# Optimization experiments

Hardware: AMD Instinct MI355X
Metric: run time of the kernel (lower is better)

Reference implementation:

```python
import jax, jax.numpy as jnp
import numpy as np

B, NP, C_IN, H = 8, 6250, 512, 256   # graphs, nodes/graph, in-feat, hidden
EPG = 100000                          # edges per graph
K = 5000                              # ceil(0.8 * NP) kept by TopKPooling
H3 = 3 * H


def setup_inputs() -> dict:
    key = jax.random.key(0)
    ks = jax.random.split(key, 16)
    N, E = B * NP, B * EPG
    x = jax.random.normal(ks[0], (N, C_IN), jnp.float32)
    offs = (jnp.arange(E) // EPG) * NP  # keep edges inside their graph
    src = jax.random.randint(ks[1], (E,), 0, NP) + offs
    dst = jax.random.randint(ks[2], (E,), 0, NP) + offs
    edge_index = jnp.stack([src, dst]).astype(jnp.int64)
    edge_attr = jax.random.uniform(ks[3], (E,), jnp.float32)
    batch = jnp.repeat(jnp.arange(B), NP).astype(jnp.int64)
    s = 0.05
    W1 = jax.random.normal(ks[4], (C_IN, H), jnp.float32) * s
    b1 = jnp.zeros((H,), jnp.float32)
    W2 = jax.random.normal(ks[5], (H, H), jnp.float32) * s
    b2 = jnp.zeros((H,), jnp.float32)
    pw = jax.random.normal(ks[6], (H3,), jnp.float32) * s   # TopKPooling attn vector
    lw1 = jax.random.normal(ks[7], (H3 * 2, H), jnp.float32) * s
    lb1 = jnp.zeros((H,), jnp.float32)
    lw2 = jax.random.normal(ks[8], (H, H // 2), jnp.float32) * s
    lb2 = jnp.zeros((H // 2,), jnp.float32)
    lw3 = jax.random.normal(ks[9], (H // 2, 3), jnp.float32) * s
    lb3 = jnp.zeros((3,), jnp.float32)
    return {"x": x, "edge_index": edge_index, "edge_attr": edge_attr, "batch": batch,
            "W1": W1, "b1": b1, "W2": W2, "b2": b2, "pw": pw,
            "lw1": lw1, "lb1": lb1, "lw2": lw2, "lb2": lb2, "lw3": lw3, "lb3": lb3}


def _gcn(x, W, b, src, dst, ew, n):
    xw = x @ W
    deg = jnp.zeros((n,), xw.dtype).at[dst].add(ew) + 1.0
    dinv = jax.lax.rsqrt(deg)
    norm = dinv[src] * ew * dinv[dst]
    out = jnp.zeros_like(xw).at[dst].add(norm[:, None] * xw[src])
    return out + (dinv * dinv)[:, None] * xw + b


def reference(x, edge_index, edge_attr, batch, W1, b1, W2, b2, pw,
              lw1, lb1, lw2, lb2, lw3, lb3):
    N = x.shape[0]
    src, dst = edge_index[0], edge_index[1]
    x1 = jax.nn.relu(_gcn(x, W1, b1, src, dst, edge_attr, N))
    x2 = jax.nn.relu(_gcn(x1, W2, b2, src, dst, edge_attr, N))
    x3 = jax.nn.relu(_gcn(x2, W2, b2, src, dst, edge_attr, N))  # conv2 reused (as in source)
    cat_x = jnp.concatenate([x1, x2, x3], axis=1)               # [N, 3H]
    # TopKPooling: score = sigmoid((x . w) / ||w||), keep top-K per graph, scale by score
    score = jax.nn.sigmoid((cat_x @ pw) / jnp.linalg.norm(pw))   # [N]
    sc = score.reshape(B, NP)
    topv, topi = jax.lax.top_k(sc, K)                            # [B, K]
    xg = cat_x.reshape(B, NP, H3)
    sel = jnp.take_along_axis(xg, topi[:, :, None], axis=1) * topv[:, :, None]  # [B, K, 3H]
    readout = jnp.concatenate([sel.mean(axis=1), sel.max(axis=1)], axis=1)      # [B, 6H]
    h = jax.nn.relu(readout @ lw1 + lb1)
    h = jax.nn.relu(h @ lw2 + lb2)       # dropout p=0 is a no-op
    return h @ lw3 + lb3                 # [B, 3]
```

## Files before the change

kernel.cpp:

```cpp
#include <hip/hip_runtime.h>
#include <stdint.h>

#define NODES  50000
#define MPAD   50048
#define NGRAPH 8
#define NP_G   6250
#define EPG    100000
#define EDGES  800000
#define KKEEP  5000
#define HID    256
#define CIN    512
#define H3     768
#define SCANB  196
#define RCHUNK 200
#define MLPCH  24
#define MLPCK  64
#define ESL    3125

#define K1_HIST  512
#define K1_W1    512
#define K1_W2    256
#define K1_TOTAL (K1_HIST + K1_W1 + K1_W2 + 1)
#define GEMM_GRID 784
#define K2_GEMM  GEMM_GRID
#define K2_FILL  256
#define K2_TOTAL (K2_GEMM + K2_FILL)

using f32x4  = __attribute__((ext_vector_type(4))) float;
using bf16x8 = __attribute__((ext_vector_type(8))) short;
using u16x8  = __attribute__((ext_vector_type(8))) unsigned short;
typedef unsigned short u16;
typedef unsigned int   u32;
typedef unsigned long long u64;

__device__ __forceinline__ float bf2f(u16 u) {
    return __uint_as_float(((uint32_t)u) << 16);
}
__device__ __forceinline__ u16 f2bf(float f) {
    uint32_t u = __float_as_uint(f);
    u += 0x7fffu + ((u >> 16) & 1u);
    return (u16)(u >> 16);
}
__device__ __forceinline__ int4 f32x8_to_bf16x8(float4 a, float4 b) {
    int4 r;
    asm("v_cvt_pk_bf16_f32 %0, %1, %2" : "=v"(r.x) : "v"(a.x), "v"(a.y));
    asm("v_cvt_pk_bf16_f32 %0, %1, %2" : "=v"(r.y) : "v"(a.z), "v"(a.w));
    asm("v_cvt_pk_bf16_f32 %0, %1, %2" : "=v"(r.z) : "v"(b.x), "v"(b.y));
    asm("v_cvt_pk_bf16_f32 %0, %1, %2" : "=v"(r.w) : "v"(b.z), "v"(b.w));
    return r;
}

__global__ __launch_bounds__(256) void k1_kernel(
        const int* __restrict__ ei, const float* __restrict__ ew,
        u64* __restrict__ partial,
        const float* __restrict__ W1, const float* __restrict__ W2,
        const float* __restrict__ pw,
        u16* __restrict__ Wt1, u16* __restrict__ Wt2, float* __restrict__ invn) {
    __shared__ __align__(16) char smem[ESL * 8];
    int b = blockIdx.x, t = threadIdx.x;
    if (b < K1_HIST) {
        u64* hl = (u64*)smem;
        int g  = b >> 6;
        int r  = b & 63;
        int bb = r >> 1;
        int h  = r & 1;
        for (int k = t; k < ESL; k += 256) hl[k] = 0ull;
        __syncthreads();
        int ebase = g * EPG + bb * ESL;
        int lo = h * ESL;
        for (int k = t; k < ESL; k += 256) {
            int e = ebase + k;
            int d = ei[EDGES + e];
            int il = d - g * NP_G - lo;
            if ((unsigned)il < (unsigned)ESL) {
                u64 enc = (1ull << 48) | (u64)(ew[e] * 4294967296.0f);
                atomicAdd(&hl[il], enc);
            }
        }
        __syncthreads();
        u64* prow = partial + (size_t)(g * 32 + bb) * NP_G + lo;
        for (int k = t; k < ESL; k += 256) prow[k] = hl[k];
    } else if (b < K1_HIST + K1_W1) {
        int id = (b - K1_HIST) * 256 + t;
        int n = id >> 9, k = id & 511;
        Wt1[id] = f2bf(W1[(size_t)k * HID + n]);
    } else if (b < K1_TOTAL - 1) {
        int id = (b - K1_HIST - K1_W1) * 256 + t;
        int n = id >> 8, k = id & 255;
        Wt2[id] = f2bf(W2[(size_t)k * HID + n]);
    } else {
        float* sh = (float*)smem;
        float s = 0.f;
        for (int i = t; i < H3; i += 256) { float v = pw[i]; s += v * v; }
        sh[t] = s; __syncthreads();
        for (int off = 128; off; off >>= 1) {
            if (t < off) sh[t] += sh[t + off];
            __syncthreads();
        }
        if (t == 0) invn[0] = rsqrtf(sh[0]);
    }
}

__global__ void scan1_kernel(const u64* __restrict__ partial,
                             u32* __restrict__ blockbase,
                             int* __restrict__ iscan, int* __restrict__ bsum,
                             float* __restrict__ dinv) {
    int b = blockIdx.x, t = threadIdx.x;
    int i = b * 256 + t;
    int c = 0;
    if (i < NODES) {
        int g = i / NP_G, il = i - g * NP_G;
        size_t base = (size_t)(g * 32) * NP_G + il;
        u64 fix = 0ull; u32 cnt = 0;
#pragma unroll 4
        for (int j = 0; j < 32; ++j) {
            size_t idx = base + (size_t)j * NP_G;
            u64 pv = partial[idx];
            blockbase[idx] = cnt;
            cnt += (u32)(pv >> 48);
            fix += pv & 0xFFFFFFFFFFFFull;
        }
        c = (int)cnt;
        float deg = (float)fix * (1.0f / 4294967296.0f);
        dinv[i] = rsqrtf(deg + 1.0f);
    }
    int lane = t & 63, wv = t >> 6;
    int v = c;
    for (int off = 1; off < 64; off <<= 1) {
        int u = __shfl_up(v, off);
        if (lane >= off) v += u;
    }
    __shared__ int ws[4];
    if (lane == 63) ws[wv] = v;
    __syncthreads();
    if (t == 0) { int s = 0; for (int k = 0; k < 4; k++) { int tmp = ws[k]; ws[k] = s; s += tmp; } }
    __syncthreads();
    v += ws[wv];
    if (i < NODES) iscan[i] = v - c;
    if (t == 255) bsum[b] = v;
}

__global__ void scan3_kernel(const int* __restrict__ iscan, const int* __restrict__ bsum,
                             int* __restrict__ rowptr) {
    int b = blockIdx.x, t = threadIdx.x;
    int v = (t < b) ? bsum[t] : 0;
    for (int off = 1; off < 64; off <<= 1) v += __shfl_xor(v, off, 64);
    __shared__ int ws[4];
    if ((t & 63) == 0) ws[t >> 6] = v;
    __syncthreads();
    int boffb = ws[0] + ws[1] + ws[2] + ws[3];
    int i = b * 256 + t;
    if (i > NODES) return;
    if (i == NODES) { rowptr[NODES] = EDGES; return; }
    rowptr[i] = boffb + iscan[i];
}

__device__ __forceinline__ bool gemm_map(int i, int& bm, int& bn) {
    int g = i & 7, s = i >> 3;
    int cnt = (g == 5) ? 48 : 49;
    if ((s >> 1) >= cnt) return false;
    bm = 49 * g - (g > 5 ? 1 : 0) + (s >> 1);
    bn = s & 1;
    return true;
}

__device__ __forceinline__ void gemm_body(const u16* __restrict__ A,
                                          const u16* __restrict__ Bt,
                                          u16* __restrict__ C,
                                          int K, int bm, int bn,
                                          u16* As, u16* Bs) {
    const int tid  = threadIdx.x;
    const int wave = tid >> 6, lane = tid & 63;
    const int wm = wave >> 1, wn = wave & 1;
    const int quad = lane >> 4, l16 = lane & 15;
    const int sr = tid >> 2;
    const int sc = tid & 3;
    const int swz = (sc ^ ((sr >> 1) & 3)) * 8;
    const int rphys = (quad ^ ((l16 >> 1) & 3)) * 8;

    const u16* Ag = A + (size_t)(bm * 128 + sr) * K + sc * 8;
    const u16* Bg = Bt + (size_t)(bn * 128 + sr) * K + sc * 8;

    f32x4 acc[4][4];
#pragma unroll
    for (int i = 0; i < 4; i++)
#pragma unroll
        for (int j = 0; j < 4; j++) { f32x4 z = {0.f, 0.f, 0.f, 0.f}; acc[i][j] = z; }

    for (int k0 = 0; k0 < K; k0 += 32) {
        int4 av0 = *(const int4*)(Ag + k0);
        int4 av1 = *(const int4*)(Ag + (size_t)64 * K + k0);
        int4 bv0 = *(const int4*)(Bg + k0);
        int4 bv1 = *(const int4*)(Bg + (size_t)64 * K + k0);
        __syncthreads();
        *(int4*)(As + sr * 32 + swz)        = av0;
        *(int4*)(As + (sr + 64) * 32 + swz) = av1;
        *(int4*)(Bs + sr * 32 + swz)        = bv0;
        *(int4*)(Bs + (sr + 64) * 32 + swz) = bv1;
        __syncthreads();
        bf16x8 af[4], bfr[4];
#pragma unroll
        for (int i = 0; i < 4; i++)
            af[i] = *(const bf16x8*)(As + (wm * 64 + i * 16 + l16) * 32 + rphys);
#pragma unroll
        for (int j = 0; j < 4; j++)
            bfr[j] = *(const bf16x8*)(Bs + (wn * 64 + j * 16 + l16) * 32 + rphys);
#pragma unroll
        for (int i = 0; i < 4; i++)
#pragma unroll
            for (int j = 0; j < 4; j++)
                acc[i][j] = __builtin_amdgcn_mfma_f32_16x16x32_bf16(af[i], bfr[j], acc[i][j], 0, 0, 0);
    }

    const int crow0 = bm * 128 + wm * 64 + quad * 4;
    const int ccol0 = bn * 128 + wn * 64 + l16;
#pragma unroll
    for (int i = 0; i < 4; i++)
#pragma unroll
        for (int j = 0; j < 4; j++)
#pragma unroll
            for (int r = 0; r < 4; r++)
                C[(size_t)(crow0 + i * 16 + r) * HID + ccol0 + j * 16] = f2bf(acc[i][j][r]);
}

__device__ __forceinline__ void gemm_body_f32A(const float* __restrict__ X,
                                               const u16* __restrict__ Bt,
                                               u16* __restrict__ C,
                                               int bm, int bn,
                                               u16* As, u16* Bs) {
    const int tid  = threadIdx.x;
    const int wave = tid >> 6, lane = tid & 63;
    const int wm = wave >> 1, wn = wave & 1;
    const int quad = lane >> 4, l16 = lane & 15;
    const int sr = tid >> 2;
    const int sc = tid & 3;
    const int swz = (sc ^ ((sr >> 1) & 3)) * 8;
    const int rphys = (quad ^ ((l16 >> 1) & 3)) * 8;

    int r0 = bm * 128 + sr;      if (r0 > NODES - 1) r0 = NODES - 1;
    int r1 = bm * 128 + sr + 64; if (r1 > NODES - 1) r1 = NODES - 1;
    const float* Ag0 = X + (size_t)r0 * CIN + sc * 8;
    const float* Ag1 = X + (size_t)r1 * CIN + sc * 8;
    const u16*   Bg  = Bt + (size_t)(bn * 128 + sr) * CIN + sc * 8;

    f32x4 acc[4][4];
#pragma unroll
    for (int i = 0; i < 4; i++)
#pragma unroll
        for (int j = 0; j < 4; j++) { f32x4 z = {0.f, 0.f, 0.f, 0.f}; acc[i][j] = z; }

    for (int k0 = 0; k0 < CIN; k0 += 32) {
        float4 a00 = *(const float4*)(Ag0 + k0);
        float4 a01 = *(const float4*)(Ag0 + k0 + 4);
        float4 a10 = *(const float4*)(Ag1 + k0);
        float4 a11 = *(const float4*)(Ag1 + k0 + 4);
        int4 bv0 = *(const int4*)(Bg + k0);
        int4 bv1 = *(const int4*)(Bg + (size_t)64 * CIN + k0);
        int4 av0 = f32x8_to_bf16x8(a00, a01);
        int4 av1 = f32x8_to_bf16x8(a10, a11);
        __syncthreads();
        *(int4*)(As + sr * 32 + swz)        = av0;
        *(int4*)(As + (sr + 64) * 32 + swz) = av1;
        *(int4*)(Bs + sr * 32 + swz)        = bv0;
        *(int4*)(Bs + (sr + 64) * 32 + swz) = bv1;
        __syncthreads();
        bf16x8 af[4], bfr[4];
#pragma unroll
        for (int i = 0; i < 4; i++)
            af[i] = *(const bf16x8*)(As + (wm * 64 + i * 16 + l16) * 32 + rphys);
#pragma unroll
        for (int j = 0; j < 4; j++)
            bfr[j] = *(const bf16x8*)(Bs + (wn * 64 + j * 16 + l16) * 32 + rphys);
#pragma unroll
        for (int i = 0; i < 4; i++)
#pragma unroll
            for (int j = 0; j < 4; j++)
                acc[i][j] = __builtin_amdgcn_mfma_f32_16x16x32_bf16(af[i], bfr[j], acc[i][j], 0, 0, 0);
    }

    const int crow0 = bm * 128 + wm * 64 + quad * 4;
    const int ccol0 = bn * 128 + wn * 64 + l16;
#pragma unroll
    for (int i = 0; i < 4; i++)
#pragma unroll
        for (int j = 0; j < 4; j++)
#pragma unroll
            for (int r = 0; r < 4; r++)
                C[(size_t)(crow0 + i * 16 + r) * HID + ccol0 + j * 16] = f2bf(acc[i][j][r]);
}

__global__ __launch_bounds__(256) void k2_kernel(
        const float* __restrict__ x, const u16* __restrict__ Wt1, u16* __restrict__ xw,
        const int* __restrict__ ei, const float* __restrict__ ew,
        const float* __restrict__ dinv, const int* __restrict__ rowptr,
        const u32* __restrict__ blockbase, int2* __restrict__ csr) {
    __shared__ __align__(16) char smem[NP_G * 4];
    int b = blockIdx.x;
    if (b < K2_GEMM) {
        int bm, bn;
        if (!gemm_map(b, bm, bn)) return;
        u16* As = (u16*)smem;
        u16* Bs = (u16*)(smem + 8192);
        gemm_body_f32A(x, Wt1, xw, bm, bn, As, Bs);
    } else {
        u32* cursor = (u32*)smem;
        int g  = b & 7;
        int bb = (b - K2_GEMM) >> 3;
        const u32* bbase = blockbase + (size_t)(g * 32 + bb) * NP_G;
        const int* rp = rowptr + g * NP_G;
        for (int k = threadIdx.x; k < NP_G; k += 256)
            cursor[k] = (u32)rp[k] + bbase[k];
        __syncthreads();
        int ebase = g * EPG + bb * ESL;
#pragma unroll 4
        for (int k = threadIdx.x; k < ESL; k += 256) {
            int e = ebase + k;
            int s = ei[e], d = ei[EDGES + e];
            int il = d - g * NP_G;
            u32 pos = atomicAdd(&cursor[il], 1u);
            csr[pos] = make_int2(s, __float_as_int(dinv[s] * ew[e] * dinv[d]));
        }
    }
}

__global__ __launch_bounds__(256) void gemm_bt(const u16* __restrict__ A,
                                               const u16* __restrict__ Bt,
                                               u16* __restrict__ C, int K) {
    __shared__ u16 As[128 * 32];
    __shared__ u16 Bs[128 * 32];
    int bm, bn;
    if (!gemm_map(blockIdx.x, bm, bn)) return;
    gemm_body(A, Bt, C, K, bm, bn, As, Bs);
}

template<bool SCORE>
__global__ void agg_kernel(const u16* __restrict__ xw, u16* __restrict__ xo,
                           const int* __restrict__ rowptr, const int2* __restrict__ csr,
                           const float* __restrict__ dinv, const float* __restrict__ bias,
                           const u16* __restrict__ xs1, const u16* __restrict__ xs2,
                           const float* __restrict__ pw, const float* __restrict__ invn,
                           float* __restrict__ score, u64* __restrict__ keys) {
    int wave = threadIdx.x >> 6;
    int lane = threadIdx.x & 63;
    int g  = blockIdx.x & 7;
    int nl = (blockIdx.x >> 3) * 4 + wave;
    if (nl >= NP_G) return;
    int w = g * NP_G + nl;
    int half = lane >> 5;
    int f8 = (lane & 31) * 8;
    size_t ro = (size_t)w * HID + f8;

    float acc0[8], acc1[8];
#pragma unroll
    for (int j = 0; j < 8; ++j) { acc0[j] = 0.f; acc1[j] = 0.f; }

    int p = rowptr[w], p1 = rowptr[w + 1];
    for (int q = p; q < p1; q += 64) {
        int m = min(64, p1 - q);
        int2 e = make_int2(0, 0);
        if (lane < m) e = csr[q + lane];
        int j = 0;
        for (; j + 16 <= m; j += 16) {
            int   s[8]; float wt[8];
#pragma unroll
            for (int k = 0; k < 8; ++k) {
                int idx = j + 2 * k + half;
                s[k]  = __shfl(e.x, idx, 64);
                wt[k] = __int_as_float(__shfl(e.y, idx, 64));
            }
            u16x8 v[8];
#pragma unroll
            for (int k = 0; k < 8; ++k)
                v[k] = *(const u16x8*)(xw + (size_t)s[k] * HID + f8);
#pragma unroll
            for (int k = 0; k < 8; k += 2) {
#pragma unroll
                for (int t = 0; t < 8; ++t) {
                    acc0[t] += wt[k]     * bf2f(v[k][t]);
                    acc1[t] += wt[k + 1] * bf2f(v[k + 1][t]);
                }
            }
        }
        for (; j + 8 <= m; j += 8) {
            int i0 = j + half,     i1 = j + 2 + half;
            int i2 = j + 4 + half, i3 = j + 6 + half;
            int   s0 = __shfl(e.x, i0, 64); float w0 = __int_as_float(__shfl(e.y, i0, 64));
            int   s1 = __shfl(e.x, i1, 64); float w1 = __int_as_float(__shfl(e.y, i1, 64));
            int   s2 = __shfl(e.x, i2, 64); float w2 = __int_as_float(__shfl(e.y, i2, 64));
            int   s3 = __shfl(e.x, i3, 64); float w3 = __int_as_float(__shfl(e.y, i3, 64));
            u16x8 v0 = *(const u16x8*)(xw + (size_t)s0 * HID + f8);
            u16x8 v1 = *(const u16x8*)(xw + (size_t)s1 * HID + f8);
            u16x8 v2 = *(const u16x8*)(xw + (size_t)s2 * HID + f8);
            u16x8 v3 = *(const u16x8*)(xw + (size_t)s3 * HID + f8);
#pragma unroll
            for (int t = 0; t < 8; ++t) {
                acc0[t] += w0 * bf2f(v0[t]);
                acc1[t] += w1 * bf2f(v1[t]);
                acc0[t] += w2 * bf2f(v2[t]);
                acc1[t] += w3 * bf2f(v3[t]);
            }
        }
        for (; j + 2 <= m; j += 2) {
            int i0 = j + half;
            int s0 = __shfl(e.x, i0, 64); float w0 = __int_as_float(__shfl(e.y, i0, 64));
            u16x8 v0 = *(const u16x8*)(xw + (size_t)s0 * HID + f8);
#pragma unroll
            for (int t = 0; t < 8; ++t) acc0[t] += w0 * bf2f(v0[t]);
        }
        if (j < m) {
            int s0 = __shfl(e.x, j, 64); float w0 = __int_as_float(__shfl(e.y, j, 64));
            w0 = half ? 0.f : w0;
            u16x8 v0 = *(const u16x8*)(xw + (size_t)s0 * HID + f8);
#pragma unroll
            for (int t = 0; t < 8; ++t) acc0[t] += w0 * bf2f(v0[t]);
        }
    }

#pragma unroll
    for (int j = 0; j < 8; ++j) {
        acc0[j] += acc1[j];
        acc0[j] += __shfl(acc0[j], lane ^ 32, 64);
    }

    float di = dinv[w], sw = di * di;
    u16x8 sv = *(const u16x8*)(xw + ro);
    float bb[8];
    {
        float4 t0 = *(const float4*)(bias + f8);
        float4 t1 = *(const float4*)(bias + f8 + 4);
        bb[0] = t0.x; bb[1] = t0.y; bb[2] = t0.z; bb[3] = t0.w;
        bb[4] = t1.x; bb[5] = t1.y; bb[6] = t1.z; bb[7] = t1.w;
    }
    u16x8 o;
    float ov[8];
#pragma unroll
    for (int j = 0; j < 8; ++j) {
        float v = fmaxf(acc0[j] + sw * bf2f(sv[j]) + bb[j], 0.f);
        o[j] = f2bf(v);
        ov[j] = bf2f(o[j]);
    }
    if (half == 0) *(u16x8*)(xo + ro) = o;

    if (SCORE) {
        u16x8 v1 = *(const u16x8*)(xs1 + ro);
        u16x8 v2 = *(const u16x8*)(xs2 + ro);
        float acc = 0.f;
#pragma unroll
        for (int j = 0; j < 8; ++j) {
            acc += bf2f(v1[j]) * pw[f8 + j];
            acc += bf2f(v2[j]) * pw[256 + f8 + j];
            acc += ov[j]       * pw[512 + f8 + j];
        }
#pragma unroll
        for (int off = 1; off < 32; off <<= 1) acc += __shfl_xor(acc, off, 64);
        if (lane == 0) {
            float s = acc * invn[0];
            float sc = 1.f / (1.f + __expf(-s));
            score[w] = sc;
            keys[w] = ((u64)__float_as_uint(sc) << 13) | (unsigned int)(NP_G - 1 - nl);
        }
    }
}

__global__ __launch_bounds__(1024) void selcomp_kernel(
        const u64* __restrict__ keys, const float* __restrict__ score,
        int* __restrict__ selidx, float* __restrict__ selscr) {
    __shared__ u64 kk[NP_G];
    __shared__ unsigned int hist[4][256];
    __shared__ unsigned int sfx[257];
    __shared__ u64 spref;
    __shared__ unsigned int swant;
    int g = blockIdx.x, t = threadIdx.x;
    const u64* kg = keys + (size_t)g * NP_G;
    for (int i = t; i < NP_G; i += 1024) kk[i] = kg[i];
    if (t == 0) { spref = 0ull; swant = KKEEP; }
    const int wgrp = (t >> 8) & 3;
    u64 mask = 0ull;
    __syncthreads();
    for (int shift = 40; shift >= 0; shift -= 8) {
        if (t < 256) { hist[0][t] = 0; hist[1][t] = 0; hist[2][t] = 0; hist[3][t] = 0; }
        __syncthreads();
        u64 pref = spref;
        for (int i = t; i < NP_G; i += 1024) {
            u64 key = kk[i];
            if ((key & mask) == pref)
                atomicAdd(&hist[wgrp][(unsigned int)(key >> shift) & 255u], 1u);
        }
        __syncthreads();
        if (t < 256) sfx[t] = hist[0][t] + hist[1][t] + hist[2][t] + hist[3][t];
        if (t == 0) sfx[256] = 0;
        __syncthreads();
        for (int off = 1; off < 256; off <<= 1) {
            unsigned int v = 0;
            if (t < 256 && t + off < 256) v = sfx[t + off];
            __syncthreads();
            if (t < 256 && t + off < 256) sfx[t] += v;
            __syncthreads();
        }
        unsigned int want = swant;
        __syncthreads();
        if (t < 256) {
            unsigned int s0 = sfx[t], s1 = sfx[t + 1];
            if (s0 >= want && s1 < want) {
                spref = pref | ((u64)t << shift);
                swant = want - s1;
            }
        }
        __syncthreads();
        mask |= (255ull << shift);
    }
    u64 kth = spref;
    int lane = t & 63, wv = t >> 6;
    __shared__ int wsum[16];
    __shared__ int cbase;
    if (t == 0) cbase = 0;
    __syncthreads();
    for (int k = 0; k < (NP_G + 1023) / 1024; ++k) {
        int i = k * 1024 + t;
        bool sel = (i < NP_G) && (kk[i] >= kth);
        int n = g * NP_G + i;
        u64 bal = __ballot(sel);
        int prefix = __popcll(bal & ((1ull << lane) - 1ull));
        if (lane == 0) wsum[wv] = __popcll(bal);
        __syncthreads();
        if (t == 0) {
            int s = cbase;
            for (int j = 0; j < 16; ++j) { int tmp = wsum[j]; wsum[j] = s; s += tmp; }
            cbase = s;
        }
        __syncthreads();
        if (sel) {
            int pos = wsum[wv] + prefix;
            selidx[g * KKEEP + pos] = n;
            selscr[g * KKEEP + pos] = score[n];
        }
        __syncthreads();
    }
}

__global__ __launch_bounds__(256) void readout_kernel(
        const u16* __restrict__ x1, const u16* __restrict__ x2,
        const u16* __restrict__ x3,
        const int* __restrict__ selidx, const float* __restrict__ selscr,
        float* __restrict__ sumbuf, int* __restrict__ maxbuf) {
    int g = blockIdx.x, tpart = blockIdx.y, c = blockIdx.z;
    int fcol = threadIdx.x;
    const u16* xt = (tpart == 0) ? x1 : ((tpart == 1) ? x2 : x3);
    __shared__ int   sidx[RCHUNK];
    __shared__ float sscr[RCHUNK];
    int base = g * KKEEP + c * RCHUNK;
    if (fcol < RCHUNK) { sidx[fcol] = selidx[base + fcol]; sscr[fcol] = selscr[base + fcol]; }
    __syncthreads();
    float sum = 0.f, mx = 0.f;
#pragma unroll 1
    for (int j = 0; j < RCHUNK; j += 4) {
        int n0 = sidx[j], n1 = sidx[j + 1], n2 = sidx[j + 2], n3 = sidx[j + 3];
        float s0 = sscr[j], s1 = sscr[j + 1], s2 = sscr[j + 2], s3 = sscr[j + 3];
        float v0 = bf2f(xt[(size_t)n0 * HID + fcol]) * s0;
        float v1 = bf2f(xt[(size_t)n1 * HID + fcol]) * s1;
        float v2 = bf2f(xt[(size_t)n2 * HID + fcol]) * s2;
        float v3 = bf2f(xt[(size_t)n3 * HID + fcol]) * s3;
        sum += v0 + v1 + v2 + v3;
        mx = fmaxf(mx, fmaxf(fmaxf(v0, v1), fmaxf(v2, v3)));
    }
    int o = (g * 3 + tpart) * HID + fcol;
    atomicAdd(&sumbuf[o], sum);
    atomicMax(&maxbuf[o], __float_as_int(mx));
}

__global__ __launch_bounds__(256) void mlp1_kernel(const float* __restrict__ sumbuf,
                                                   const int* __restrict__ maxbuf,
                                                   const float* __restrict__ lw1,
                                                   float* __restrict__ h1acc) {
    int g = blockIdx.x, ch = blockIdx.y, t = threadIdx.x;
    __shared__ float r[MLPCK];
    int k0 = ch * MLPCK;
    if (t < MLPCK) {
        int i = k0 + t;
        r[t] = (i < 768) ? sumbuf[g * 768 + i] * (1.f / 5000.f)
                         : __int_as_float(maxbuf[g * 768 + (i - 768)]);
    }
    __syncthreads();
    float a0 = 0.f, a1 = 0.f, a2 = 0.f, a3 = 0.f;
#pragma unroll
    for (int i = 0; i < MLPCK; i += 4) {
        a0 += r[i]     * lw1[(size_t)(k0 + i)     * 256 + t];
        a1 += r[i + 1] * lw1[(size_t)(k0 + i + 1) * 256 + t];
        a2 += r[i + 2] * lw1[(size_t)(k0 + i + 2) * 256 + t];
        a3 += r[i + 3] * lw1[(size_t)(k0 + i + 3) * 256 + t];
    }
    atomicAdd(&h1acc[g * 256 + t], (a0 + a1) + (a2 + a3));
}

__global__ __launch_bounds__(256) void mlp2_kernel(const float* __restrict__ h1acc,
                                                   const float* __restrict__ lb1,
                                                   const float* __restrict__ lw2,
                                                   const float* __restrict__ lb2,
                                                   const float* __restrict__ lw3,
                                                   const float* __restrict__ lb3,
                                                   float* __restrict__ out) {
    __shared__ float h1[256];
    __shared__ float part[256];
    __shared__ float h2[128];
    int g = blockIdx.x, t = threadIdx.x;
    h1[t] = fmaxf(h1acc[g * 256 + t] + lb1[t], 0.f);
    __syncthreads();
    int col = t & 127, half = t >> 7;
    float a = 0.f;
#pragma unroll
    for (int i = 0; i < 128; i += 4) {
        int k = half * 128 + i;
        a += h1[k]     * lw2[k * 128 + col]
           + h1[k + 1] * lw2[(k + 1) * 128 + col]
           + h1[k + 2] * lw2[(k + 2) * 128 + col]
           + h1[k + 3] * lw2[(k + 3) * 128 + col];
    }
    part[t] = a;
    __syncthreads();
    if (t < 128) h2[t] = fmaxf(part[t] + part[t + 128] + lb2[t], 0.f);
    __syncthreads();
    if (t < 3) {
        float a3 = lb3[t];
        for (int i = 0; i < 128; ++i) a3 += h2[i] * lw3[i * 3 + t];
        out[g * 3 + t] = a3;
    }
}

extern "C" void kernel_launch(void* const* d_in, const int* in_sizes, int n_in,
                              void* d_out, int out_size, void* d_ws, size_t ws_size,
                              hipStream_t stream) {
    const float* x   = (const float*)d_in[0];
    const int*   ei  = (const int*)d_in[1];
    const float* ew  = (const float*)d_in[2];
    const float* W1  = (const float*)d_in[4];
    const float* b1  = (const float*)d_in[5];
    const float* W2  = (const float*)d_in[6];
    const float* b2  = (const float*)d_in[7];
    const float* pw  = (const float*)d_in[8];
    const float* lw1 = (const float*)d_in[9];
    const float* lb1 = (const float*)d_in[10];
    const float* lw2 = (const float*)d_in[11];
    const float* lb2 = (const float*)d_in[12];
    const float* lw3 = (const float*)d_in[13];
    const float* lb3 = (const float*)d_in[14];
    float* out = (float*)d_out;

    char* p = (char*)d_ws;
    auto alloc = [&](size_t bytes) -> char* {
        char* r = p;
        p += (bytes + 255) & ~(size_t)255;
        return r;
    };
    u16* A0  = (u16*)alloc((size_t)MPAD * CIN * 2);
    u16* x3  = (u16*)alloc((size_t)MPAD * HID * 2);
    u16* xw  = (u16*)alloc((size_t)MPAD * HID * 2);
    u16* Wt1 = (u16*)alloc((size_t)HID * CIN * 2);
    u16* Wt2 = (u16*)alloc((size_t)HID * HID * 2);
    int2*  csr    = (int2*)alloc((size_t)EDGES * 8);
    u64*   partial   = (u64*)alloc((size_t)256 * NP_G * 8);
    u32*   blockbase = (u32*)alloc((size_t)256 * NP_G * 4);
    int*   rowptr = (int*)alloc((size_t)(NODES + 1) * 4);
    int*   iscan  = (int*)alloc((size_t)NODES * 4);
    int*   bsum   = (int*)alloc((size_t)SCANB * 4);
    u64*   keys   = (u64*)alloc((size_t)NODES * 8);
    float* score  = (float*)alloc((size_t)NODES * 4);
    float* dinv   = (float*)alloc((size_t)NODES * 4);
    int*   selidx = (int*)alloc((size_t)NGRAPH * KKEEP * 4);
    float* selscr = (float*)alloc((size_t)NGRAPH * KKEEP * 4);
    float* invn   = (float*)alloc(256);
    char* zbase = p;
    float* sumbuf = (float*)alloc(6144 * 4);
    int*   maxbuf = (int*)alloc(6144 * 4);
    float* h1acc  = (float*)alloc((size_t)NGRAPH * 256 * 4);
    size_t zbytes = (size_t)(p - zbase);

    u16* x1 = A0;
    u16* x2 = A0 + (size_t)MPAD * HID;

    hipMemsetAsync(zbase, 0, zbytes, stream);

    k1_kernel<<<K1_TOTAL, 256, 0, stream>>>(ei, ew, partial,
                                            W1, W2, pw, Wt1, Wt2, invn);
    scan1_kernel<<<SCANB, 256, 0, stream>>>(partial, blockbase, iscan, bsum, dinv);
    scan3_kernel<<<SCANB + 1, 256, 0, stream>>>(iscan, bsum, rowptr);
    k2_kernel<<<K2_TOTAL, 256, 0, stream>>>(x, Wt1, xw, ei, ew, dinv, rowptr,
                                            blockbase, csr);

    int aggBlocks = 8 * ((NP_G + 3) / 4);

    agg_kernel<false><<<aggBlocks, 256, 0, stream>>>(xw, x1, rowptr, csr, dinv, b1,
                                                     nullptr, nullptr, nullptr, nullptr,
                                                     nullptr, nullptr);
    gemm_bt<<<GEMM_GRID, 256, 0, stream>>>(x1, Wt2, xw, HID);
    agg_kernel<false><<<aggBlocks, 256, 0, stream>>>(xw, x2, rowptr, csr, dinv, b2,
                                                     nullptr, nullptr, nullptr, nullptr,
                                                     nullptr, nullptr);
    gemm_bt<<<GEMM_GRID, 256, 0, stream>>>(x2, Wt2, xw, HID);
    agg_kernel<true><<<aggBlocks, 256, 0, stream>>>(xw, x3, rowptr, csr, dinv, b2,
                                                    x1, x2, pw, invn, score, keys);

    selcomp_kernel<<<NGRAPH, 1024, 0, stream>>>(keys, score, selidx, selscr);
    readout_kernel<<<dim3(NGRAPH, 3, KKEEP / RCHUNK), 256, 0, stream>>>(
        x1, x2, x3, selidx, selscr, sumbuf, maxbuf);
    mlp1_kernel<<<dim3(NGRAPH, MLPCH), 256, 0, stream>>>(sumbuf, maxbuf, lw1, h1acc);
    mlp2_kernel<<<NGRAPH, 256, 0, stream>>>(h1acc, lb1, lw2, lb2, lw3, lb3, out);
}
```

Before: 472.7 us.

## Split fused GEMM/CSR-fill kernel and halve fill shared memory; drop 16-edge agg unroll

The first GEMM and the CSR fill no longer share one launch. The GEMM becomes its own kernel needing only 16KB of shared memory. The fill becomes a separate kernel whose per-node cursor array is halved, so it processes the destination range in two passes, rescanning edges each pass. This lowers per-block shared memory in both kernels for better occupancy, at the cost of an extra launch, lost overlap between GEMM and fill, and double edge reads in the fill. The 16-edge unrolled loop in the aggregation kernel is also removed, which reduces register pressure but gives up memory-level parallelism.

```diff
diff --git a/kernel.cpp b/kernel.cpp
--- a/kernel.cpp
+++ b/kernel.cpp
@@ -22,9 +22,7 @@
 #define K1_W2    256
 #define K1_TOTAL (K1_HIST + K1_W1 + K1_W2 + 1)
 #define GEMM_GRID 784
-#define K2_GEMM  GEMM_GRID
-#define K2_FILL  256
-#define K2_TOTAL (K2_GEMM + K2_FILL)
+#define FILL_GRID 256
 
 using f32x4  = __attribute__((ext_vector_type(4))) float;
 using bf16x8 = __attribute__((ext_vector_type(8))) short;
@@ -223,11 +221,14 @@
                 C[(size_t)(crow0 + i * 16 + r) * HID + ccol0 + j * 16] = f2bf(acc[i][j][r]);
 }
 
-__device__ __forceinline__ void gemm_body_f32A(const float* __restrict__ X,
-                                               const u16* __restrict__ Bt,
-                                               u16* __restrict__ C,
-                                               int bm, int bn,
-                                               u16* As, u16* Bs) {
+__global__ __launch_bounds__(256) void k2_kernel(
+        const float* __restrict__ X, const u16* __restrict__ Wt1,
+        u16* __restrict__ C) {
+    __shared__ u16 As[128 * 32];
+    __shared__ u16 Bs[128 * 32];
+    int bm, bn;
+    if (!gemm_map(blockIdx.x, bm, bn)) return;
+
     const int tid  = threadIdx.x;
     const int wave = tid >> 6, lane = tid & 63;
     const int wm = wave >> 1, wn = wave & 1;
@@ -241,7 +242,7 @@
     int r1 = bm * 128 + sr + 64; if (r1 > NODES - 1) r1 = NODES - 1;
     const float* Ag0 = X + (size_t)r0 * CIN + sc * 8;
     const float* Ag1 = X + (size_t)r1 * CIN + sc * 8;
-    const u16*   Bg  = Bt + (size_t)(bn * 128 + sr) * CIN + sc * 8;
+    const u16*   Bg  = Wt1 + (size_t)(bn * 128 + sr) * CIN + sc * 8;
 
     f32x4 acc[4][4];
 #pragma unroll
@@ -289,37 +290,33 @@
                 C[(size_t)(crow0 + i * 16 + r) * HID + ccol0 + j * 16] = f2bf(acc[i][j][r]);
 }
 
-__global__ __launch_bounds__(256) void k2_kernel(
-        const float* __restrict__ x, const u16* __restrict__ Wt1, u16* __restrict__ xw,
+__global__ __launch_bounds__(256) void fill_kernel(
         const int* __restrict__ ei, const float* __restrict__ ew,
         const float* __restrict__ dinv, const int* __restrict__ rowptr,
         const u32* __restrict__ blockbase, int2* __restrict__ csr) {
-    __shared__ __align__(16) char smem[NP_G * 4];
-    int b = blockIdx.x;
-    if (b < K2_GEMM) {
-        int bm, bn;
-        if (!gemm_map(b, bm, bn)) return;
-        u16* As = (u16*)smem;
-        u16* Bs = (u16*)(smem + 8192);
-        gemm_body_f32A(x, Wt1, xw, bm, bn, As, Bs);
-    } else {
-        u32* cursor = (u32*)smem;
-        int g  = b & 7;
-        int bb = (b - K2_GEMM) >> 3;
-        const u32* bbase = blockbase + (size_t)(g * 32 + bb) * NP_G;
-        const int* rp = rowptr + g * NP_G;
-        for (int k = threadIdx.x; k < NP_G; k += 256)
-            cursor[k] = (u32)rp[k] + bbase[k];
-        __syncthreads();
-        int ebase = g * EPG + bb * ESL;
+    __shared__ u32 cursor[ESL];
+    int g  = blockIdx.x & 7;
+    int bb = blockIdx.x >> 3;
+    const u32* bbase = blockbase + (size_t)(g * 32 + bb) * NP_G;
+    const int* rp = rowptr + g * NP_G;
+    int ebase = g * EPG + bb * ESL;
+    for (int h = 0; h < 2; ++h) {
+        int lo = h * ESL;
+        for (int k = threadIdx.x; k < ESL; k += 256)
+            cursor[k] = (u32)rp[lo + k] + bbase[lo + k];
+        __syncthreads();
 #pragma unroll 4
         for (int k = threadIdx.x; k < ESL; k += 256) {
             int e = ebase + k;
-            int s = ei[e], d = ei[EDGES + e];
-            int il = d - g * NP_G;
-            u32 pos = atomicAdd(&cursor[il], 1u);
-            csr[pos] = make_int2(s, __float_as_int(dinv[s] * ew[e] * dinv[d]));
-        }
+            int d = ei[EDGES + e];
+            int il = d - g * NP_G - lo;
+            if ((unsigned)il < (unsigned)ESL) {
+                int s = ei[e];
+                u32 pos = atomicAdd(&cursor[il], 1u);
+                csr[pos] = make_int2(s, __float_as_int(dinv[s] * ew[e] * dinv[d]));
+            }
+        }
+        __syncthreads();
     }
 }
 
@@ -360,27 +357,6 @@
         int2 e = make_int2(0, 0);
         if (lane < m) e = csr[q + lane];
         int j = 0;
-        for (; j + 16 <= m; j += 16) {
-            int   s[8]; float wt[8];
-#pragma unroll
-            for (int k = 0; k < 8; ++k) {
-                int idx = j + 2 * k + half;
-                s[k]  = __shfl(e.x, idx, 64);
-                wt[k] = __int_as_float(__shfl(e.y, idx, 64));
-            }
-            u16x8 v[8];
-#pragma unroll
-            for (int k = 0; k < 8; ++k)
-                v[k] = *(const u16x8*)(xw + (size_t)s[k] * HID + f8);
-#pragma unroll
-            for (int k = 0; k < 8; k += 2) {
-#pragma unroll
-                for (int t = 0; t < 8; ++t) {
-                    acc0[t] += wt[k]     * bf2f(v[k][t]);
-                    acc1[t] += wt[k + 1] * bf2f(v[k + 1][t]);
-                }
-            }
-        }
         for (; j + 8 <= m; j += 8) {
             int i0 = j + half,     i1 = j + 2 + half;
             int i2 = j + 4 + half, i3 = j + 6 + half;
@@ -683,8 +659,8 @@
                                             W1, W2, pw, Wt1, Wt2, invn);
     scan1_kernel<<<SCANB, 256, 0, stream>>>(partial, blockbase, iscan, bsum, dinv);
     scan3_kernel<<<SCANB + 1, 256, 0, stream>>>(iscan, bsum, rowptr);
-    k2_kernel<<<K2_TOTAL, 256, 0, stream>>>(x, Wt1, xw, ei, ew, dinv, rowptr,
-                                            blockbase, csr);
+    k2_kernel<<<GEMM_GRID, 256, 0, stream>>>(x, Wt1, xw);
+    fill_kernel<<<FILL_GRID, 256, 0, stream>>>(ei, ew, dinv, rowptr, blockbase, csr);
 
     int aggBlocks = 8 * ((NP_G + 3) / 4);
 
```

New measurement: 475.7 us. No clear change (+0.6%).
